# Optimization experiments

Hardware: AMD Instinct MI355X
Metric: run time of the kernel (lower is better)

The kernel has to match this reference:

```python
import jax, jax.numpy as jnp
import numpy as np

N_NODES = 100000
N_EDGES = 1600000
IN_CH = 128
OUT_CH = 128
N_REL = 8


def setup_inputs() -> dict:
    key = jax.random.key(0)
    k1, k2, k3, k4, k5, k6 = jax.random.split(key, 6)
    x = jax.random.normal(k1, (N_NODES, IN_CH), dtype=jnp.float32)
    edge_index = jax.random.randint(k2, (2, N_EDGES), 0, N_NODES, dtype=jnp.int64)
    edge_type = jax.random.randint(k3, (N_EDGES,), 0, N_REL, dtype=jnp.int64)
    # learned parameters (PyG RGCNConv: per-relation weight, root weight, bias)
    scale = 1.0 / np.sqrt(IN_CH)
    weight = jax.random.normal(k4, (N_REL, IN_CH, OUT_CH), dtype=jnp.float32) * scale
    root = jax.random.normal(k5, (IN_CH, OUT_CH), dtype=jnp.float32) * scale
    bias = jax.random.normal(k6, (OUT_CH,), dtype=jnp.float32) * 0.01
    return {"x": x, "edge_index": edge_index, "edge_type": edge_type,
            "weight": weight, "root": root, "bias": bias}


def reference(x, edge_index, edge_type, weight, root, bias):
    # PyG RGCNConv forward: out_i = x_i @ root + bias
    #   + sum_r mean_{j in N_r(i)} (x_j @ W_r)   (default aggr='mean' per relation)
    N = x.shape[0]
    R, _, O = weight.shape
    src, dst = edge_index[0], edge_index[1]
    # transform all nodes under every relation once: [R, N, O]
    xW = jnp.einsum('ni,rio->rno', x, weight)
    msg = xW[edge_type, src]                      # [E, O] per-edge message
    seg = edge_type * N + dst                     # segment per (relation, dst)
    sums = jax.ops.segment_sum(msg, seg, num_segments=R * N)        # [R*N, O]
    cnt = jax.ops.segment_sum(jnp.ones_like(msg[:, 0]), seg, num_segments=R * N)
    mean = sums / jnp.maximum(cnt, 1.0)[:, None]
    agg = mean.reshape(R, N, O).sum(axis=0)       # sum over relations
    return agg + x @ root + bias
```

## Files before the change

### kernel.cpp

```cpp
#include <hip/hip_runtime.h>
#include <hip/hip_bf16.h>
#include <stdint.h>

#define N_NODES 100000
#define N_EDGES 1600000
#define CH 128
#define N_REL 8
#define N_PAD 100096
#define N_KEYS (N_NODES * N_REL)

#define NBKT 782
#define NCHUNK 782
#define CHUNK_E 2048
#define OFFS_STRIDE 784
#define PERM_LDS_CAP 4096

using frag_ab = __attribute__((ext_vector_type(8))) short;
using frag_cd = __attribute__((ext_vector_type(4))) float;

__device__ __forceinline__ short f2bs(float f) {
    union { __hip_bfloat16 h; short s; } u;
    u.h = __float2bfloat16(f);
    return u.s;
}

__device__ __forceinline__ uint32_t pack2bf(float a, float b) {
    union { __hip_bfloat16 h; unsigned short s; } ua, ub;
    ua.h = __float2bfloat16(a); ub.h = __float2bfloat16(b);
    return (uint32_t)ua.s | ((uint32_t)ub.s << 16);
}

__device__ __forceinline__ float bf_lo(uint32_t u) { return __uint_as_float(u << 16); }
__device__ __forceinline__ float bf_hi(uint32_t u) { return __uint_as_float(u & 0xffff0000u); }


__global__ __launch_bounds__(256)
void prep_kernel(const int* __restrict__ ei, const int* __restrict__ et,
                 uint32_t* __restrict__ ents, int* __restrict__ offs,
                 const float* __restrict__ root, const float* __restrict__ W,
                 short* __restrict__ Bsw) {
    __shared__ uint32_t esave[CHUNK_E];
    __shared__ uint32_t csave[CHUNK_E];
    __shared__ short bsave[CHUNK_E];
    __shared__ int cnt[NBKT];
    __shared__ int scan_t[256];
    const int tid = threadIdx.x;
    const int c = blockIdx.x;
    const int g = blockIdx.x * 256 + tid;

    if (g < 9 * 2048) {
        int chunk = g >> 11, entry = g & 2047;
        int m16 = entry & 15, ct = (entry >> 4) & 7, quad = (entry >> 7) & 3, ks = entry >> 9;
        const float* src = (chunk == 0) ? root : W + (size_t)(chunk - 1) * CH * CH;
        int col = ct * 16 + m16, kb = ks * 32 + quad * 8;
        frag_ab f;
#pragma unroll
        for (int j = 0; j < 8; ++j) f[j] = f2bs(src[(size_t)(kb + j) * CH + col]);
        *(frag_ab*)(Bsw + (size_t)g * 8) = f;
    }

    for (int i = tid; i < NBKT; i += 256) cnt[i] = 0;
    __syncthreads();
#pragma unroll
    for (int j = 0; j < 8; ++j) {
        const int li = j * 256 + tid;
        const int e = c * CHUNK_E + li;
        if (e < N_EDGES) {
            const int dst = ei[N_EDGES + e];
            const int src = ei[e];
            const int r = et[e];
            const int b = dst >> 7;
            atomicAdd(&cnt[b], 1);
            esave[li] = ((uint32_t)src << 10) | ((uint32_t)(dst & 127) << 3) | (uint32_t)r;
            bsave[li] = (short)b;
        } else {
            bsave[li] = -1;
        }
    }
    __syncthreads();
    const int b4 = 4 * tid;
    int c0 = (b4 < NBKT) ? cnt[b4] : 0;
    int c1 = (b4 + 1 < NBKT) ? cnt[b4 + 1] : 0;
    int c2 = (b4 + 2 < NBKT) ? cnt[b4 + 2] : 0;
    int c3 = (b4 + 3 < NBKT) ? cnt[b4 + 3] : 0;
    const int s4 = c0 + c1 + c2 + c3;
    scan_t[tid] = s4;
    __syncthreads();
    for (int st = 1; st < 256; st <<= 1) {
        int u = (tid >= st) ? scan_t[tid - st] : 0;
        __syncthreads();
        scan_t[tid] += u;
        __syncthreads();
    }
    const int excl = scan_t[tid] - s4;
    const int total = scan_t[255];
    {
        const int o0 = excl, o1 = o0 + c0, o2 = o1 + c1, o3 = o2 + c2;
        int* og = offs + (size_t)c * OFFS_STRIDE;
        if (b4 < NBKT)     { cnt[b4]     = o0; og[b4]     = o0; }
        if (b4 + 1 < NBKT) { cnt[b4 + 1] = o1; og[b4 + 1] = o1; }
        if (b4 + 2 < NBKT) { cnt[b4 + 2] = o2; og[b4 + 2] = o2; }
        if (b4 + 3 < NBKT) { cnt[b4 + 3] = o3; og[b4 + 3] = o3; }
        if (tid == 0) og[NBKT] = total;
    }
    __syncthreads();
#pragma unroll
    for (int j = 0; j < 8; ++j) {
        const int li = j * 256 + tid;
        const int b = bsave[li];
        if (b >= 0) {
            const int pos = atomicAdd(&cnt[b], 1);
            csave[pos] = esave[li];
        }
    }
    __syncthreads();
    {
        const uint4* cs = (const uint4*)csave;
        uint4* dg = (uint4*)(ents + (size_t)c * CHUNK_E);
#pragma unroll
        for (int i = 0; i < 2; ++i) dg[tid + 256 * i] = cs[tid + 256 * i];
    }
}


__global__ __launch_bounds__(512)
void bin_kernel(const uint32_t* __restrict__ ents, const int* __restrict__ offs,
                int* __restrict__ perm_g, int* __restrict__ ends_g,
                const float* __restrict__ x, short* __restrict__ xb) {
    __shared__ uint32_t stage[PERM_LDS_CAP];
    __shared__ int soff[NCHUNK];
    __shared__ int slen[NCHUNK];
    __shared__ int sbase[NCHUNK];
    __shared__ int hist[1024];
    __shared__ int cursor[1024];
    __shared__ int shl[512];
    const int tid = threadIdx.x;
    const int b = blockIdx.x;

    {
        const int nst = NBKT * 512;
        const float4* xp = (const float4*)x;
        for (int gi = b * 512 + tid; gi < N_NODES * CH / 8; gi += nst) {
            float4 a = xp[(size_t)gi * 2], bb = xp[(size_t)gi * 2 + 1];
            frag_ab f;
            f[0] = f2bs(a.x); f[1] = f2bs(a.y); f[2] = f2bs(a.z); f[3] = f2bs(a.w);
            f[4] = f2bs(bb.x); f[5] = f2bs(bb.y); f[6] = f2bs(bb.z); f[7] = f2bs(bb.w);
            *(frag_ab*)(xb + (size_t)gi * 8) = f;
        }
    }

    for (int c = tid; c < NCHUNK; c += 512) {
        const int s = offs[(size_t)c * OFFS_STRIDE + b];
        const int e = offs[(size_t)c * OFFS_STRIDE + b + 1];
        soff[c] = s;
        slen[c] = e - s;
    }
    hist[tid] = 0; hist[tid + 512] = 0;
    __syncthreads();
    {
        const int t2 = 2 * tid;
        const int h0 = (t2 < NCHUNK) ? slen[t2] : 0;
        const int h1 = (t2 + 1 < NCHUNK) ? slen[t2 + 1] : 0;
        const int s2 = h0 + h1;
        shl[tid] = s2;
        __syncthreads();
        for (int st = 1; st < 512; st <<= 1) {
            int u = (tid >= st) ? shl[tid - st] : 0;
            __syncthreads();
            shl[tid] += u;
            __syncthreads();
        }
        const int excl = shl[tid] - s2;
        if (t2 < NCHUNK)     sbase[t2]     = excl;
        if (t2 + 1 < NCHUNK) sbase[t2 + 1] = excl + h0;
    }
    __syncthreads();
#pragma unroll
    for (int k = 0; k < 2; ++k) {
        const int c = 2 * tid + k;
        if (c < NCHUNK) {
            const int s = soff[c], n_c = slen[c], base = sbase[c];
            const uint32_t* src = ents + (size_t)c * CHUNK_E + s;
            for (int i = 0; i < n_c; ++i) {
                const int pos = base + i;
                if (pos < PERM_LDS_CAP) stage[pos] = src[i];
            }
        }
    }
    __syncthreads();
    int n = shl[511];
    if (n > PERM_LDS_CAP) n = PERM_LDS_CAP;
    for (int i = tid; i < n; i += 512) atomicAdd(&hist[stage[i] & 1023], 1);
    __syncthreads();
    const int h0 = hist[2 * tid], h1 = hist[2 * tid + 1];
    const int s2 = h0 + h1;
    shl[tid] = s2;
    __syncthreads();
    for (int st = 1; st < 512; st <<= 1) {
        int u = (tid >= st) ? shl[tid - st] : 0;
        __syncthreads();
        shl[tid] += u;
        __syncthreads();
    }
    const int excl = shl[tid] - s2;
    cursor[2 * tid]     = excl;
    cursor[2 * tid + 1] = excl + h0;
    {
        int e1 = excl + h0, e2 = excl + h0 + h1;
        ends_g[(size_t)b * 1024 + 2 * tid]     = (e1 > PERM_LDS_CAP) ? PERM_LDS_CAP : e1;
        ends_g[(size_t)b * 1024 + 2 * tid + 1] = (e2 > PERM_LDS_CAP) ? PERM_LDS_CAP : e2;
    }
    __syncthreads();
    for (int i = tid; i < n; i += 512) {
        const uint32_t v = stage[i];
        const int pos = atomicAdd(&cursor[v & 1023], 1);
        if (pos < PERM_LDS_CAP) perm_g[(size_t)b * PERM_LDS_CAP + pos] = (int)(v >> 10);
    }
}

#define ACC_U4(U, B)                                            \
    do {                                                        \
        a[(B)+0] += bf_lo((U).x); a[(B)+1] += bf_hi((U).x);     \
        a[(B)+2] += bf_lo((U).y); a[(B)+3] += bf_hi((U).y);     \
        a[(B)+4] += bf_lo((U).z); a[(B)+5] += bf_hi((U).z);     \
        a[(B)+6] += bf_lo((U).w); a[(B)+7] += bf_hi((U).w);     \
    } while (0)

__global__ __launch_bounds__(512, 4)
void rgcn_fused(const int* __restrict__ ends_g, const int* __restrict__ perm_g,
                const short* __restrict__ xb, const short* __restrict__ Bsw,
                const float* __restrict__ bias, float* __restrict__ out) {
    __shared__ short Ash[128 * 128];
    __shared__ int perm_lds[PERM_LDS_CAP];
    __shared__ int lends[1025];
    const int tid = threadIdx.x;
    const int wave = tid >> 6, lane = tid & 63;
    const int m16 = lane & 15, quad = lane >> 4;
    const int wm = wave >> 2, wn = wave & 3;
    const int b = blockIdx.x;
    const long B0 = (long)b * 128;

    if (tid == 0) { lends[0] = 0; perm_lds[0] = 0; }
    for (int i = tid; i < 1024; i += 512) lends[1 + i] = ends_g[(size_t)b * 1024 + i];
    __syncthreads();
    const int nperm = lends[1024];
    for (int i = tid; i < nperm; i += 512) perm_lds[i] = perm_g[(size_t)b * PERM_LDS_CAP + i];

    float bcol[2];
#pragma unroll
    for (int ct = 0; ct < 2; ++ct) bcol[ct] = bias[wn * 32 + ct * 16 + m16];

    frag_cd acc[4][2];
#pragma unroll
    for (int mt = 0; mt < 4; ++mt)
#pragma unroll
        for (int ct = 0; ct < 2; ++ct) acc[mt][ct] = (frag_cd){0.f, 0.f, 0.f, 0.f};

#pragma unroll
    for (int ks = 0; ks < 4; ++ks) {
        frag_ab af[4];
#pragma unroll
        for (int mt = 0; mt < 4; ++mt)
            af[mt] = *(const frag_ab*)(xb + (B0 + wm * 64 + mt * 16 + m16) * CH + ks * 32 + quad * 8);
#pragma unroll
        for (int ct = 0; ct < 2; ++ct) {
            frag_ab bf = *(const frag_ab*)(Bsw + (size_t)((((ks * 4 + quad) * 8) + wn * 2 + ct) * 16 + m16) * 8);
#pragma unroll
            for (int mt = 0; mt < 4; ++mt)
                acc[mt][ct] = __builtin_amdgcn_mfma_f32_16x16x32_bf16(af[mt], bf, acc[mt][ct], 0, 0, 0);
        }
    }
    __syncthreads();

    const int lrow = tid >> 2;
    const int q4 = tid & 3;
    const uint32_t ch64 = (uint32_t)q4 << 6;
    const char* xbp = (const char*)xb;
    char* drow = (char*)Ash + lrow * 256;
    const int swz = lrow & 7;

    for (int r = 0; r < N_REL; ++r) {
        const int keyL = lrow * 8 + r;
        const int s = lends[keyL];
        const int e = lends[keyL + 1];
        float a[32];
#pragma unroll
        for (int i = 0; i < 32; ++i) a[i] = 0.f;
        int p0 = perm_lds[(s < e) ? s : 0];
        int p1 = perm_lds[(s + 1 < e) ? s + 1 : ((s < e) ? s : 0)];
        for (int k = s; k < e; k += 2) {
            const char* c0 = xbp + (((size_t)(uint32_t)p0 << 8) | ch64);
            const char* c1 = xbp + (((size_t)(uint32_t)p1 << 8) | ch64);
            const uint4 u0 = *(const uint4*)(c0);
            const uint4 u1 = *(const uint4*)(c0 + 16);
            const uint4 u2 = *(const uint4*)(c0 + 32);
            const uint4 u3 = *(const uint4*)(c0 + 48);
            const uint4 u4 = *(const uint4*)(c1);
            const uint4 u5 = *(const uint4*)(c1 + 16);
            const uint4 u6 = *(const uint4*)(c1 + 32);
            const uint4 u7 = *(const uint4*)(c1 + 48);
            const bool two = (k + 1 < e);
            const int kn = k + 2;
            p0 = perm_lds[(kn < e) ? kn : 0];
            p1 = perm_lds[(kn + 1 < e) ? kn + 1 : 0];
            ACC_U4(u0, 0); ACC_U4(u1, 8); ACC_U4(u2, 16); ACC_U4(u3, 24);
            if (two) { ACC_U4(u4, 0); ACC_U4(u5, 8); ACC_U4(u6, 16); ACC_U4(u7, 24); }
        }
        const int c = e - s;
        const float sc = (c > 1) ? (1.0f / (float)c) : 1.0f;
#pragma unroll
        for (int t = 0; t < 4; ++t) {
            uint4 w;
            w.x = pack2bf(a[t * 8 + 0] * sc, a[t * 8 + 1] * sc);
            w.y = pack2bf(a[t * 8 + 2] * sc, a[t * 8 + 3] * sc);
            w.z = pack2bf(a[t * 8 + 4] * sc, a[t * 8 + 5] * sc);
            w.w = pack2bf(a[t * 8 + 6] * sc, a[t * 8 + 7] * sc);
            *(uint4*)(drow + (((q4 * 4 + t) ^ swz) << 4)) = w;
        }
        __syncthreads();
        const short* Bc = Bsw + (size_t)(r + 1) * 2048 * 8;
#pragma unroll
        for (int ks = 0; ks < 4; ++ks) {
            frag_ab af[4];
#pragma unroll
            for (int mt = 0; mt < 4; ++mt) {
                const int lr = wm * 64 + mt * 16 + m16;
                af[mt] = *(const frag_ab*)((const char*)Ash + lr * 256 + (((ks * 4 + quad) ^ (lr & 7)) << 4));
            }
#pragma unroll
            for (int ct = 0; ct < 2; ++ct) {
                frag_ab bf = *(const frag_ab*)(Bc + (size_t)((((ks * 4 + quad) * 8) + wn * 2 + ct) * 16 + m16) * 8);
#pragma unroll
                for (int mt = 0; mt < 4; ++mt)
                    acc[mt][ct] = __builtin_amdgcn_mfma_f32_16x16x32_bf16(af[mt], bf, acc[mt][ct], 0, 0, 0);
            }
        }
        __syncthreads();
    }

#pragma unroll
    for (int mt = 0; mt < 4; ++mt) {
#pragma unroll
        for (int ct = 0; ct < 2; ++ct) {
            const long row0 = B0 + wm * 64 + mt * 16 + quad * 4;
            const int col = wn * 32 + ct * 16 + m16;
#pragma unroll
            for (int rg = 0; rg < 4; ++rg) {
                const long rr = row0 + rg;
                if (rr < N_NODES) out[rr * CH + col] = acc[mt][ct][rg] + bcol[ct];
            }
        }
    }
}


__global__ void count_rd_kernel(const int* __restrict__ ei, const int* __restrict__ et,
                                int* __restrict__ cnt) {
    int e = blockIdx.x * 256 + threadIdx.x;
    if (e < N_EDGES) {
        int dst = ei[N_EDGES + e];
        int r = et[e];
        atomicAdd(&cnt[r * N_NODES + dst], 1);
    }
}

__global__ void scatter_kernel(const int* __restrict__ ei, const int* __restrict__ et,
                               const float* __restrict__ x, float* __restrict__ sums,
                               int rel) {
    int gid = (blockIdx.x * 256 + threadIdx.x) >> 5;
    int lane = threadIdx.x & 31;
    int ngroups = gridDim.x * 8;
    for (int e = gid; e < N_EDGES; e += ngroups) {
        if (et[e] != rel) continue;
        int src = ei[e];
        int dst = ei[N_EDGES + e];
        float4 v = ((const float4*)(x + (size_t)src * CH))[lane];
        float* s = sums + (size_t)dst * CH + (size_t)lane * 4;
        atomicAdd(s + 0, v.x);
        atomicAdd(s + 1, v.y);
        atomicAdd(s + 2, v.z);
        atomicAdd(s + 3, v.w);
    }
}

__global__ __launch_bounds__(256, 2)
void gemm_kernel(const float* __restrict__ A, const float* __restrict__ B,
                 const float* __restrict__ bias, const int* __restrict__ cnt,
                 float* __restrict__ out, int accumulate) {
    const int wave = threadIdx.x >> 6;
    const int lane = threadIdx.x & 63;
    const int m16 = lane & 15;
    const int quad = lane >> 4;

    frag_ab bfrag[4][8];
#pragma unroll
    for (int ks = 0; ks < 4; ++ks) {
        const int kb = ks * 32 + quad * 8;
#pragma unroll
        for (int ct = 0; ct < 8; ++ct) {
            const int col = ct * 16 + m16;
            frag_ab f;
#pragma unroll
            for (int j = 0; j < 8; ++j)
                f[j] = f2bs(B[(size_t)(kb + j) * CH + col]);
            bfrag[ks][ct] = f;
        }
    }

    const int nstrips = (N_NODES + 63) / 64;
    for (int strip = blockIdx.x; strip < nstrips; strip += gridDim.x) {
        const int row = strip * 64 + wave * 16 + m16;
        const bool valid = row < N_NODES;
        float scale = 1.0f;
        if (cnt != nullptr && valid) {
            int c = cnt[row];
            if (c > 1) scale = 1.0f / (float)c;
        }
        const float4* arow = (const float4*)(A + (size_t)(valid ? row : 0) * CH);
        frag_cd acc[8];
#pragma unroll
        for (int ct = 0; ct < 8; ++ct) acc[ct] = (frag_cd){0.f, 0.f, 0.f, 0.f};
#pragma unroll
        for (int ks = 0; ks < 4; ++ks) {
            float4 a0 = arow[ks * 8 + quad * 2];
            float4 a1 = arow[ks * 8 + quad * 2 + 1];
            frag_ab af;
            af[0] = f2bs(a0.x * scale); af[1] = f2bs(a0.y * scale);
            af[2] = f2bs(a0.z * scale); af[3] = f2bs(a0.w * scale);
            af[4] = f2bs(a1.x * scale); af[5] = f2bs(a1.y * scale);
            af[6] = f2bs(a1.z * scale); af[7] = f2bs(a1.w * scale);
#pragma unroll
            for (int ct = 0; ct < 8; ++ct)
                acc[ct] = __builtin_amdgcn_mfma_f32_16x16x32_bf16(af, bfrag[ks][ct], acc[ct], 0, 0, 0);
        }
        const int obase = strip * 64 + wave * 16 + quad * 4;
#pragma unroll
        for (int ct = 0; ct < 8; ++ct) {
            const int col = ct * 16 + m16;
#pragma unroll
            for (int rg = 0; rg < 4; ++rg) {
                const int r = obase + rg;
                if (r < N_NODES) {
                    const size_t idx = (size_t)r * CH + col;
                    if (accumulate) out[idx] += acc[ct][rg];
                    else out[idx] = acc[ct][rg] + bias[col];
                }
            }
        }
    }
}

__global__ void edge_transform_kernel(const int* __restrict__ ei, const int* __restrict__ et,
                                      const float* __restrict__ x, const float* __restrict__ W,
                                      const int* __restrict__ cnt, float* __restrict__ out) {
    __shared__ float xs[CH];
    const int tid = threadIdx.x;
    for (int e = blockIdx.x; e < N_EDGES; e += gridDim.x) {
        const int src = ei[e];
        const int dst = ei[N_EDGES + e];
        const int r = et[e];
        __syncthreads();
        xs[tid] = x[(size_t)src * CH + tid];
        __syncthreads();
        const int c = cnt[r * N_NODES + dst];
        const float scale = (c > 1) ? (1.0f / (float)c) : 1.0f;
        const float* Wr = W + (size_t)r * CH * CH;
        float acc = 0.f;
#pragma unroll 8
        for (int k = 0; k < CH; ++k) acc += xs[k] * Wr[(size_t)k * CH + tid];
        atomicAdd(&out[(size_t)dst * CH + tid], acc * scale);
    }
}


static inline size_t al512(size_t x) { return (x + 511) & ~(size_t)511; }

extern "C" void kernel_launch(void* const* d_in, const int* in_sizes, int n_in,
                              void* d_out, int out_size, void* d_ws, size_t ws_size,
                              hipStream_t stream) {
    const float* x    = (const float*)d_in[0];
    const int*   ei   = (const int*)d_in[1];
    const int*   et   = (const int*)d_in[2];
    const float* W    = (const float*)d_in[3];
    const float* root = (const float*)d_in[4];
    const float* bias = (const float*)d_in[5];
    float* out = (float*)d_out;

    size_t o = 0;
    const size_t o_ents = o; o += al512((size_t)NCHUNK * CHUNK_E * 4);
    const size_t o_offs = o; o += al512((size_t)NCHUNK * OFFS_STRIDE * 4);
    const size_t o_perm = o; o += al512((size_t)NBKT * PERM_LDS_CAP * 4);
    const size_t o_ends = o; o += al512((size_t)NBKT * 1024 * 4);
    const size_t o_bsw  = o; o += al512((size_t)9 * 2048 * 16);
    const size_t o_xb   = o; o += al512((size_t)N_PAD * CH * 2);
    const size_t need_t1 = o;

    const size_t cnt_bytes = (size_t)N_REL * N_NODES * sizeof(int);
    const size_t cnt_rsv   = al512(cnt_bytes);
    const size_t sums51    = (size_t)N_NODES * CH * sizeof(float);

    char* ws = (char*)d_ws;
    if (ws_size >= need_t1) {
        uint32_t* ents   = (uint32_t*)(ws + o_ents);
        int*      offs   = (int*)(ws + o_offs);
        int*      perm_g = (int*)(ws + o_perm);
        int*      ends_g = (int*)(ws + o_ends);
        short*    Bsw    = (short*)(ws + o_bsw);
        short*    xb     = (short*)(ws + o_xb);

        prep_kernel<<<NCHUNK, 256, 0, stream>>>(ei, et, ents, offs, root, W, Bsw);
        bin_kernel<<<NBKT, 512, 0, stream>>>(ents, offs, perm_g, ends_g, x, xb);
        rgcn_fused<<<NBKT, 512, 0, stream>>>(ends_g, perm_g, xb, Bsw, bias, out);
    } else if (ws_size >= cnt_rsv + sums51) {
        int*   cnt  = (int*)d_ws;
        float* sums = (float*)((char*)d_ws + cnt_rsv);
        hipMemsetAsync(cnt, 0, cnt_bytes, stream);
        count_rd_kernel<<<(N_EDGES + 255) / 256, 256, 0, stream>>>(ei, et, cnt);
        gemm_kernel<<<512, 256, 0, stream>>>(x, root, bias, nullptr, out, 0);
        for (int r = 0; r < N_REL; ++r) {
            hipMemsetAsync(sums, 0, sums51, stream);
            scatter_kernel<<<6400, 256, 0, stream>>>(ei, et, x, sums, r);
            gemm_kernel<<<512, 256, 0, stream>>>(sums, W + (size_t)r * CH * CH,
                                                 nullptr, cnt + (size_t)r * N_NODES, out, 1);
        }
    } else {
        int* cnt = (int*)d_ws;
        hipMemsetAsync(cnt, 0, cnt_bytes, stream);
        count_rd_kernel<<<(N_EDGES + 255) / 256, 256, 0, stream>>>(ei, et, cnt);
        gemm_kernel<<<512, 256, 0, stream>>>(x, root, bias, nullptr, out, 0);
        edge_transform_kernel<<<65536, CH, 0, stream>>>(ei, et, x, W, cnt, out);
    }
}
```

Before: 270.1 us.

## Fuse bucket binning into main kernel and move x conversion to prep

Removes the separate bin_kernel. The per-bucket gather, histogram and counting sort of edges now run at the start of rgcn_fused, writing the permutation straight into LDS, which drops the global perm/ends round trip and one launch. The x-to-bf16 conversion moves into prep_kernel. In exchange, the main kernel gains extra LDS (aliased onto Ash) and a serial prologue, which may lower occupancy and add latency before the MFMA work starts.

```diff
diff --git a/kernel.cpp b/kernel.cpp
--- a/kernel.cpp
+++ b/kernel.cpp
@@ -37,6 +37,7 @@
 __global__ __launch_bounds__(256)
 void prep_kernel(const int* __restrict__ ei, const int* __restrict__ et,
                  uint32_t* __restrict__ ents, int* __restrict__ offs,
+                 const float* __restrict__ x, short* __restrict__ xb,
                  const float* __restrict__ root, const float* __restrict__ W,
                  short* __restrict__ Bsw) {
     __shared__ uint32_t esave[CHUNK_E];
@@ -57,6 +58,18 @@
 #pragma unroll
         for (int j = 0; j < 8; ++j) f[j] = f2bs(src[(size_t)(kb + j) * CH + col]);
         *(frag_ab*)(Bsw + (size_t)g * 8) = f;
+    }
+
+    {
+        const int nst = NCHUNK * 256;
+        const float4* xp = (const float4*)x;
+        for (int gi = g; gi < N_NODES * CH / 8; gi += nst) {
+            float4 a = xp[(size_t)gi * 2], bb = xp[(size_t)gi * 2 + 1];
+            frag_ab f;
+            f[0] = f2bs(a.x); f[1] = f2bs(a.y); f[2] = f2bs(a.z); f[3] = f2bs(a.w);
+            f[4] = f2bs(bb.x); f[5] = f2bs(bb.y); f[6] = f2bs(bb.z); f[7] = f2bs(bb.w);
+            *(frag_ab*)(xb + (size_t)gi * 8) = f;
+        }
     }
 
     for (int i = tid; i < NBKT; i += 256) cnt[i] = 0;
@@ -122,102 +135,6 @@
     }
 }
 
-
-__global__ __launch_bounds__(512)
-void bin_kernel(const uint32_t* __restrict__ ents, const int* __restrict__ offs,
-                int* __restrict__ perm_g, int* __restrict__ ends_g,
-                const float* __restrict__ x, short* __restrict__ xb) {
-    __shared__ uint32_t stage[PERM_LDS_CAP];
-    __shared__ int soff[NCHUNK];
-    __shared__ int slen[NCHUNK];
-    __shared__ int sbase[NCHUNK];
-    __shared__ int hist[1024];
-    __shared__ int cursor[1024];
-    __shared__ int shl[512];
-    const int tid = threadIdx.x;
-    const int b = blockIdx.x;
-
-    {
-        const int nst = NBKT * 512;
-        const float4* xp = (const float4*)x;
-        for (int gi = b * 512 + tid; gi < N_NODES * CH / 8; gi += nst) {
-            float4 a = xp[(size_t)gi * 2], bb = xp[(size_t)gi * 2 + 1];
-            frag_ab f;
-            f[0] = f2bs(a.x); f[1] = f2bs(a.y); f[2] = f2bs(a.z); f[3] = f2bs(a.w);
-            f[4] = f2bs(bb.x); f[5] = f2bs(bb.y); f[6] = f2bs(bb.z); f[7] = f2bs(bb.w);
-            *(frag_ab*)(xb + (size_t)gi * 8) = f;
-        }
-    }
-
-    for (int c = tid; c < NCHUNK; c += 512) {
-        const int s = offs[(size_t)c * OFFS_STRIDE + b];
-        const int e = offs[(size_t)c * OFFS_STRIDE + b + 1];
-        soff[c] = s;
-        slen[c] = e - s;
-    }
-    hist[tid] = 0; hist[tid + 512] = 0;
-    __syncthreads();
-    {
-        const int t2 = 2 * tid;
-        const int h0 = (t2 < NCHUNK) ? slen[t2] : 0;
-        const int h1 = (t2 + 1 < NCHUNK) ? slen[t2 + 1] : 0;
-        const int s2 = h0 + h1;
-        shl[tid] = s2;
-        __syncthreads();
-        for (int st = 1; st < 512; st <<= 1) {
-            int u = (tid >= st) ? shl[tid - st] : 0;
-            __syncthreads();
-            shl[tid] += u;
-            __syncthreads();
-        }
-        const int excl = shl[tid] - s2;
-        if (t2 < NCHUNK)     sbase[t2]     = excl;
-        if (t2 + 1 < NCHUNK) sbase[t2 + 1] = excl + h0;
-    }
-    __syncthreads();
-#pragma unroll
-    for (int k = 0; k < 2; ++k) {
-        const int c = 2 * tid + k;
-        if (c < NCHUNK) {
-            const int s = soff[c], n_c = slen[c], base = sbase[c];
-            const uint32_t* src = ents + (size_t)c * CHUNK_E + s;
-            for (int i = 0; i < n_c; ++i) {
-                const int pos = base + i;
-                if (pos < PERM_LDS_CAP) stage[pos] = src[i];
-            }
-        }
-    }
-    __syncthreads();
-    int n = shl[511];
-    if (n > PERM_LDS_CAP) n = PERM_LDS_CAP;
-    for (int i = tid; i < n; i += 512) atomicAdd(&hist[stage[i] & 1023], 1);
-    __syncthreads();
-    const int h0 = hist[2 * tid], h1 = hist[2 * tid + 1];
-    const int s2 = h0 + h1;
-    shl[tid] = s2;
-    __syncthreads();
-    for (int st = 1; st < 512; st <<= 1) {
-        int u = (tid >= st) ? shl[tid - st] : 0;
-        __syncthreads();
-        shl[tid] += u;
-        __syncthreads();
-    }
-    const int excl = shl[tid] - s2;
-    cursor[2 * tid]     = excl;
-    cursor[2 * tid + 1] = excl + h0;
-    {
-        int e1 = excl + h0, e2 = excl + h0 + h1;
-        ends_g[(size_t)b * 1024 + 2 * tid]     = (e1 > PERM_LDS_CAP) ? PERM_LDS_CAP : e1;
-        ends_g[(size_t)b * 1024 + 2 * tid + 1] = (e2 > PERM_LDS_CAP) ? PERM_LDS_CAP : e2;
-    }
-    __syncthreads();
-    for (int i = tid; i < n; i += 512) {
-        const uint32_t v = stage[i];
-        const int pos = atomicAdd(&cursor[v & 1023], 1);
-        if (pos < PERM_LDS_CAP) perm_g[(size_t)b * PERM_LDS_CAP + pos] = (int)(v >> 10);
-    }
-}
-
 #define ACC_U4(U, B)                                            \
     do {                                                        \
         a[(B)+0] += bf_lo((U).x); a[(B)+1] += bf_hi((U).x);     \
@@ -227,12 +144,20 @@
     } while (0)
 
 __global__ __launch_bounds__(512, 4)
-void rgcn_fused(const int* __restrict__ ends_g, const int* __restrict__ perm_g,
+void rgcn_fused(const uint32_t* __restrict__ ents, const int* __restrict__ offs,
                 const short* __restrict__ xb, const short* __restrict__ Bsw,
                 const float* __restrict__ bias, float* __restrict__ out) {
     __shared__ short Ash[128 * 128];
     __shared__ int perm_lds[PERM_LDS_CAP];
     __shared__ int lends[1025];
+    __shared__ int soff[NCHUNK];
+    __shared__ int slen[NCHUNK];
+    __shared__ int sbase[NCHUNK];
+    uint32_t* stage  = (uint32_t*)Ash;
+    int*      hist   = (int*)Ash + 4096;
+    int*      cursor = (int*)Ash + 5120;
+    int*      shl    = (int*)Ash + 6144;
+
     const int tid = threadIdx.x;
     const int wave = tid >> 6, lane = tid & 63;
     const int m16 = lane & 15, quad = lane >> 4;
@@ -240,11 +165,76 @@
     const int b = blockIdx.x;
     const long B0 = (long)b * 128;
 
-    if (tid == 0) { lends[0] = 0; perm_lds[0] = 0; }
-    for (int i = tid; i < 1024; i += 512) lends[1 + i] = ends_g[(size_t)b * 1024 + i];
-    __syncthreads();
-    const int nperm = lends[1024];
-    for (int i = tid; i < nperm; i += 512) perm_lds[i] = perm_g[(size_t)b * PERM_LDS_CAP + i];
+    for (int c = tid; c < NCHUNK; c += 512) {
+        const int s = offs[(size_t)c * OFFS_STRIDE + b];
+        const int e = offs[(size_t)c * OFFS_STRIDE + b + 1];
+        soff[c] = s;
+        slen[c] = e - s;
+    }
+    hist[tid] = 0; hist[tid + 512] = 0;
+    if (tid == 0) perm_lds[0] = 0;
+    __syncthreads();
+    int n_tot;
+    {
+        const int t2 = 2 * tid;
+        const int l0 = (t2 < NCHUNK) ? slen[t2] : 0;
+        const int l1 = (t2 + 1 < NCHUNK) ? slen[t2 + 1] : 0;
+        const int ls = l0 + l1;
+        shl[tid] = ls;
+        __syncthreads();
+        for (int st = 1; st < 512; st <<= 1) {
+            int u = (tid >= st) ? shl[tid - st] : 0;
+            __syncthreads();
+            shl[tid] += u;
+            __syncthreads();
+        }
+        const int lexcl = shl[tid] - ls;
+        if (t2 < NCHUNK)     sbase[t2]     = lexcl;
+        if (t2 + 1 < NCHUNK) sbase[t2 + 1] = lexcl + l0;
+        __syncthreads();
+        n_tot = shl[511];
+        if (n_tot > PERM_LDS_CAP) n_tot = PERM_LDS_CAP;
+    }
+#pragma unroll
+    for (int k = 0; k < 2; ++k) {
+        const int c = 2 * tid + k;
+        if (c < NCHUNK) {
+            const int s = soff[c], nc = slen[c], base = sbase[c];
+            const uint32_t* srcp = ents + (size_t)c * CHUNK_E + s;
+            for (int i = 0; i < nc; ++i) {
+                const int pos = base + i;
+                if (pos < PERM_LDS_CAP) stage[pos] = srcp[i];
+            }
+        }
+    }
+    __syncthreads();
+    for (int i = tid; i < n_tot; i += 512) atomicAdd(&hist[stage[i] & 1023], 1);
+    __syncthreads();
+    {
+        const int h0 = hist[2 * tid], h1 = hist[2 * tid + 1];
+        const int s2 = h0 + h1;
+        shl[tid] = s2;
+        __syncthreads();
+        for (int st = 1; st < 512; st <<= 1) {
+            int u = (tid >= st) ? shl[tid - st] : 0;
+            __syncthreads();
+            shl[tid] += u;
+            __syncthreads();
+        }
+        const int excl = shl[tid] - s2;
+        cursor[2 * tid]     = excl;
+        cursor[2 * tid + 1] = excl + h0;
+        if (tid == 0) lends[0] = 0;
+        int e1 = excl + h0, e2 = excl + h0 + h1;
+        lends[1 + 2 * tid] = (e1 > PERM_LDS_CAP) ? PERM_LDS_CAP : e1;
+        lends[2 + 2 * tid] = (e2 > PERM_LDS_CAP) ? PERM_LDS_CAP : e2;
+    }
+    __syncthreads();
+    for (int i = tid; i < n_tot; i += 512) {
+        const uint32_t v = stage[i];
+        const int pos = atomicAdd(&cursor[v & 1023], 1);
+        if (pos < PERM_LDS_CAP) perm_lds[pos] = (int)(v >> 10);
+    }
 
     float bcol[2];
 #pragma unroll
@@ -489,8 +479,6 @@
     size_t o = 0;
     const size_t o_ents = o; o += al512((size_t)NCHUNK * CHUNK_E * 4);
     const size_t o_offs = o; o += al512((size_t)NCHUNK * OFFS_STRIDE * 4);
-    const size_t o_perm = o; o += al512((size_t)NBKT * PERM_LDS_CAP * 4);
-    const size_t o_ends = o; o += al512((size_t)NBKT * 1024 * 4);
     const size_t o_bsw  = o; o += al512((size_t)9 * 2048 * 16);
     const size_t o_xb   = o; o += al512((size_t)N_PAD * CH * 2);
     const size_t need_t1 = o;
@@ -501,16 +489,13 @@
 
     char* ws = (char*)d_ws;
     if (ws_size >= need_t1) {
-        uint32_t* ents   = (uint32_t*)(ws + o_ents);
-        int*      offs   = (int*)(ws + o_offs);
-        int*      perm_g = (int*)(ws + o_perm);
-        int*      ends_g = (int*)(ws + o_ends);
-        short*    Bsw    = (short*)(ws + o_bsw);
-        short*    xb     = (short*)(ws + o_xb);
-
-        prep_kernel<<<NCHUNK, 256, 0, stream>>>(ei, et, ents, offs, root, W, Bsw);
-        bin_kernel<<<NBKT, 512, 0, stream>>>(ents, offs, perm_g, ends_g, x, xb);
-        rgcn_fused<<<NBKT, 512, 0, stream>>>(ends_g, perm_g, xb, Bsw, bias, out);
+        uint32_t* ents = (uint32_t*)(ws + o_ents);
+        int*      offs = (int*)(ws + o_offs);
+        short*    Bsw  = (short*)(ws + o_bsw);
+        short*    xb   = (short*)(ws + o_xb);
+
+        prep_kernel<<<NCHUNK, 256, 0, stream>>>(ei, et, ents, offs, x, xb, root, W, Bsw);
+        rgcn_fused<<<NBKT, 512, 0, stream>>>(ents, offs, xb, Bsw, bias, out);
     } else if (ws_size >= cnt_rsv + sums51) {
         int*   cnt  = (int*)d_ws;
         float* sums = (float*)((char*)d_ws + cnt_rsv);
```

Result: no change. 266.7 us (-1.3%).
